# Performance work log

Measured on AMD Instinct MI355X. Metric: run time of the kernel, lower is better.

The kernel has to match this reference:

```python
import jax, jax.numpy as jnp
import numpy as np

DIM = 512
NUM_HEADS = 8


def setup_inputs() -> dict:
    key = jax.random.key(0)
    k1, k2, k3, k4, k5 = jax.random.split(key, 5)
    B, N, C = 4, 4096, DIM
    x = jax.random.normal(k1, (B, N, C), dtype=jnp.float32)
    # Conv1d kernel_size=1 weights, squeezed to [out, in]
    qkv_w = jax.random.normal(k2, (3 * C, C), dtype=jnp.float32) * (C ** -0.5)
    qkv_b = jax.random.normal(k3, (3 * C,), dtype=jnp.float32) * 0.02
    out_w = jax.random.normal(k4, (C, C), dtype=jnp.float32) * (C ** -0.5)
    out_b = jax.random.normal(k5, (C,), dtype=jnp.float32) * 0.02
    return {"x": x, "qkv_w": qkv_w, "qkv_b": qkv_b, "out_w": out_w, "out_b": out_b}


def reference(x, qkv_w, qkv_b, out_w, out_b):
    B, N, C = x.shape
    H = NUM_HEADS
    hd = C // H
    scale = hd ** -0.5
    # 1x1 Conv1d == per-position linear: [B,N,C] x [3C,C] -> [B,N,3C]
    qkv = jnp.einsum('bnc,oc->bno', x, qkv_w) + qkv_b
    qkv = qkv.reshape(B, N, 3, H, hd)
    q, k, v = qkv[:, :, 0], qkv[:, :, 1], qkv[:, :, 2]  # each [B,N,H,hd]
    # NOTE: faithful to the original: q @ k.transpose(-2,-1) contracts head_dim
    # giving an [B,N,H,H] score matrix (attention across heads per position).
    scores = jnp.einsum('bnhd,bngd->bnhg', q, k) * scale
    attn = jax.nn.softmax(scores, axis=-1)
    out = jnp.einsum('bnhg,bngd->bnhd', attn, v)  # [B,N,H,hd]
    # Faithful to original: transpose(1,2) then reshape(B,N,C) interleaves axes.
    out = out.transpose(0, 2, 1, 3).reshape(B, N, C)
    out = jnp.einsum('bnc,oc->bno', out, out_w) + out_b
    return out
```

## Files before the change

kernel.cpp:

```cpp
#include <hip/hip_runtime.h>
#include <hip/hip_bf16.h>

#define DIMC 512
#define SEQ 4096
#define M_TOK 16384
#define N_QKV 1536

typedef __bf16 bfv8 __attribute__((ext_vector_type(8)));
typedef float f32v4 __attribute__((ext_vector_type(4)));
typedef unsigned short u16v8 __attribute__((ext_vector_type(8)));

static __device__ __forceinline__ float bf2f(unsigned short u) {
    union { unsigned int i; float f; } x; x.i = ((unsigned int)u) << 16; return x.f;
}
static __device__ __forceinline__ unsigned short f2bf(float f) {
    union { float f; unsigned int i; } x; x.f = f;
    unsigned int r = x.i + 0x7FFFu + ((x.i >> 16) & 1u);
    return (unsigned short)(r >> 16);
}

static __device__ __forceinline__ void gload_lds16(const void* g, void* s) {
    __builtin_amdgcn_global_load_lds(
        (const __attribute__((address_space(1))) unsigned int*)g,
        (__attribute__((address_space(3))) unsigned int*)s, 16, 0, 0);
}

#define NX8  (M_TOK * DIMC / 8)
#define NWQ8 (N_QKV * DIMC / 8)
#define NWO8 (DIMC * DIMC / 8)
__global__ __launch_bounds__(256) void cvt_all(
    const float* __restrict__ x,  const float* __restrict__ wq,
    const float* __restrict__ wo, unsigned short* __restrict__ xb,
    unsigned short* __restrict__ wqb, unsigned short* __restrict__ wob)
{
    int i = blockIdx.x * 256 + threadIdx.x;
    const float* src; unsigned short* dst; int off;
    if (i < NX8)             { src = x;  dst = xb;  off = i; }
    else if (i < NX8 + NWQ8) { src = wq; dst = wqb; off = i - NX8; }
    else                     { src = wo; dst = wob; off = i - NX8 - NWQ8; }
    const float4* p = (const float4*)src + (size_t)off * 2;
    float4 a = p[0], b = p[1];
    u16v8 o;
    o[0] = f2bf(a.x); o[1] = f2bf(a.y); o[2] = f2bf(a.z); o[3] = f2bf(a.w);
    o[4] = f2bf(b.x); o[5] = f2bf(b.y); o[6] = f2bf(b.z); o[7] = f2bf(b.w);
    *(u16v8*)(dst + (size_t)off * 8) = o;
}

template<bool OUT_BF16>
__global__ __launch_bounds__(256) void gemm_nt_2ph(
    const unsigned short* __restrict__ A,
    const unsigned short* __restrict__ B,
    const float* __restrict__ bias,
    void* __restrict__ Cout,
    int M, int N, int K)
{
    __shared__ __align__(16) unsigned short As[2][128 * 32];
    __shared__ __align__(16) unsigned short Bs[2][128 * 32];
    const int tid  = threadIdx.x;
    const int lane = tid & 63;
    const int wid  = tid >> 6;
    const int wm   = wid >> 1;
    const int wn   = wid & 1;
    const int m0 = blockIdx.x * 128;
    const int n0 = blockIdx.y * 128;
    const int frow = lane & 15;
    const int fcol = (lane >> 4) * 8;
    const int NT = K >> 5;

    f32v4 acc[4][4] = {};

    const unsigned short* aSrc[2];
    const unsigned short* bSrc[2];
    #pragma unroll
    for (int s = 0; s < 2; ++s) {
        const int p   = (s * 256 + tid) * 8;
        const int row = p >> 5;
        const int col = (p & 31) ^ (((row >> 1) & 3) << 3);
        aSrc[s] = A + (size_t)(m0 + row) * K + col;
        bSrc[s] = B + (size_t)(n0 + row) * K + col;
    }
    const int dstOff[2] = { wid * 512, 2048 + wid * 512 };

#define STAGE(kt, buf)                                                         \
    {                                                                          \
        _Pragma("unroll") for (int s = 0; s < 2; ++s) {                        \
            gload_lds16(aSrc[s] + (kt) * 32, &As[buf][dstOff[s]]);             \
            gload_lds16(bSrc[s] + (kt) * 32, &Bs[buf][dstOff[s]]);             \
        }                                                                      \
    }

    STAGE(0, 0)
    __syncthreads();

    for (int t = 0; t < NT; ++t) {
        const int p = t & 1;
        if (t + 1 < NT) STAGE(t + 1, p ^ 1)
        bfv8 af[4], bf[4];
        #pragma unroll
        for (int i = 0; i < 4; ++i) {
            const int r = wm * 64 + i * 16 + frow;
            af[i] = *(const bfv8*)(&As[p][r * 32 + (fcol ^ (((r >> 1) & 3) << 3))]);
        }
        #pragma unroll
        for (int j = 0; j < 4; ++j) {
            const int r = wn * 64 + j * 16 + frow;
            bf[j] = *(const bfv8*)(&Bs[p][r * 32 + (fcol ^ (((r >> 1) & 3) << 3))]);
        }
        #pragma unroll
        for (int i = 0; i < 4; ++i)
            #pragma unroll
            for (int j = 0; j < 4; ++j)
                acc[i][j] = __builtin_amdgcn_mfma_f32_16x16x32_bf16(
                    af[i], bf[j], acc[i][j], 0, 0, 0);
        __syncthreads();
    }
#undef STAGE

    const int erow = (lane >> 4) * 4;
    const int ecol = lane & 15;
    #pragma unroll
    for (int j = 0; j < 4; ++j) {
        const int col = n0 + wn * 64 + j * 16 + ecol;
        const float bv = bias[col];
        #pragma unroll
        for (int i = 0; i < 4; ++i) {
            const int rbase = m0 + wm * 64 + i * 16 + erow;
            #pragma unroll
            for (int r = 0; r < 4; ++r) {
                const float v = acc[i][j][r] + bv;
                if constexpr (OUT_BF16)
                    ((unsigned short*)Cout)[(size_t)(rbase + r) * N + col] = f2bf(v);
                else
                    ((float*)Cout)[(size_t)(rbase + r) * N + col] = v;
            }
        }
    }
}

__global__ __launch_bounds__(256) void attn_mix2(
    const unsigned short* __restrict__ Y1,
    unsigned short* __restrict__ Y2)
{
    const int tid  = threadIdx.x;
    const int tok  = blockIdx.x * 16 + (tid >> 4);
    const int l16  = tid & 15;
    const int h    = l16 >> 1;
    const int half = l16 & 1;
    const unsigned short* qkv = Y1 + (size_t)tok * N_QKV;

    float qf[32];
    #pragma unroll
    for (int c = 0; c < 4; ++c) {
        u16v8 v = *(const u16v8*)(qkv + h * 64 + half * 32 + c * 8);
        #pragma unroll
        for (int j = 0; j < 8; ++j) qf[c * 8 + j] = bf2f(v[j]);
    }
    float sc[8];
    #pragma unroll
    for (int g = 0; g < 8; ++g) {
        const unsigned short* kp = qkv + DIMC + g * 64 + half * 32;
        float a = 0.f;
        #pragma unroll
        for (int c = 0; c < 4; ++c) {
            u16v8 v = *(const u16v8*)(kp + c * 8);
            #pragma unroll
            for (int j = 0; j < 8; ++j) a = fmaf(qf[c * 8 + j], bf2f(v[j]), a);
        }
        a += __shfl_xor(a, 1);
        sc[g] = a * 0.125f;
    }
    float mx = sc[0];
    #pragma unroll
    for (int g = 1; g < 8; ++g) mx = fmaxf(mx, sc[g]);
    float sum = 0.f;
    #pragma unroll
    for (int g = 0; g < 8; ++g) { sc[g] = __expf(sc[g] - mx); sum += sc[g]; }
    const float inv = 1.f / sum;
    #pragma unroll
    for (int g = 0; g < 8; ++g) sc[g] *= inv;

    float o[32] = {};
    #pragma unroll
    for (int g = 0; g < 8; ++g) {
        const unsigned short* vp = qkv + 2 * DIMC + g * 64 + half * 32;
        #pragma unroll
        for (int c = 0; c < 4; ++c) {
            u16v8 v = *(const u16v8*)(vp + c * 8);
            #pragma unroll
            for (int j = 0; j < 8; ++j) o[c * 8 + j] = fmaf(sc[g], bf2f(v[j]), o[c * 8 + j]);
        }
    }
    const int n = tok & (SEQ - 1);
    const int b = tok >> 12;
    const size_t drow = (size_t)b * SEQ + h * 512 + (n >> 3);
    unsigned short* dst = Y2 + drow * DIMC + ((n & 7) << 6) + half * 32;
    #pragma unroll
    for (int c = 0; c < 4; ++c) {
        u16v8 ov;
        #pragma unroll
        for (int j = 0; j < 8; ++j) ov[j] = f2bf(o[c * 8 + j]);
        *(u16v8*)(dst + c * 8) = ov;
    }
}

extern "C" void kernel_launch(void* const* d_in, const int* in_sizes, int n_in,
                              void* d_out, int out_size, void* d_ws, size_t ws_size,
                              hipStream_t stream) {
    const float* x     = (const float*)d_in[0];
    const float* qkv_w = (const float*)d_in[1];
    const float* qkv_b = (const float*)d_in[2];
    const float* out_w = (const float*)d_in[3];
    const float* out_b = (const float*)d_in[4];
    float* out = (float*)d_out;

    unsigned short* Y1 = (unsigned short*)d_ws;
    unsigned short* Xb = Y1 + (size_t)M_TOK * N_QKV;
    unsigned short* Y2 = Xb;
    unsigned short* Wq = Xb + (size_t)M_TOK * DIMC;
    unsigned short* Wo = Wq + (size_t)N_QKV * DIMC;

    cvt_all<<<(NX8 + NWQ8 + NWO8) / 256, 256, 0, stream>>>(x, qkv_w, out_w, Xb, Wq, Wo);

    gemm_nt_2ph<true><<<dim3(M_TOK / 128, N_QKV / 128), 256, 0, stream>>>(
        Xb, Wq, qkv_b, Y1, M_TOK, N_QKV, DIMC);

    attn_mix2<<<M_TOK / 16, 256, 0, stream>>>(Y1, Y2);

    gemm_nt_2ph<false><<<dim3(M_TOK / 128, DIMC / 128), 256, 0, stream>>>(
        Y2, Wo, out_b, out, M_TOK, DIMC, DIMC);
}
```

Before: 83.98 us.

## Use 128x256 GEMM tiles with 512 threads and triple-buffered LDS pipeline

Widens each GEMM block to a 128x256 output tile with 8 waves, which raises B-tile reuse per A load. The double-buffered LDS loop becomes a three-slot ring that prefetches two k-steps ahead. The full __syncthreads is replaced by explicit vmcnt/lgkmcnt waits plus s_barrier, so global-to-LDS loads overlap MFMA work. In exchange it uses more LDS per block and launches fewer blocks (the out-projection grid shrinks to 256 blocks), which risks lower occupancy and poorer load balance.

```diff
diff --git a/kernel.cpp b/kernel.cpp
--- a/kernel.cpp
+++ b/kernel.cpp
@@ -9,6 +9,9 @@
 typedef __bf16 bfv8 __attribute__((ext_vector_type(8)));
 typedef float f32v4 __attribute__((ext_vector_type(4)));
 typedef unsigned short u16v8 __attribute__((ext_vector_type(8)));
+
+#define VMCNT(n) asm volatile("s_waitcnt vmcnt(" #n ")" ::: "memory")
+#define LGKM0()  asm volatile("s_waitcnt lgkmcnt(0)" ::: "memory")
 
 static __device__ __forceinline__ float bf2f(unsigned short u) {
     union { unsigned int i; float f; } x; x.i = ((unsigned int)u) << 16; return x.f;
@@ -47,72 +50,78 @@
 }
 
 template<bool OUT_BF16>
-__global__ __launch_bounds__(256) void gemm_nt_2ph(
+__global__ __launch_bounds__(512) void gemm_nt_r3(
     const unsigned short* __restrict__ A,
     const unsigned short* __restrict__ B,
     const float* __restrict__ bias,
     void* __restrict__ Cout,
     int M, int N, int K)
 {
-    __shared__ __align__(16) unsigned short As[2][128 * 32];
-    __shared__ __align__(16) unsigned short Bs[2][128 * 32];
+    __shared__ __align__(16) unsigned short As[3][128 * 32];
+    __shared__ __align__(16) unsigned short Bs[3][256 * 32];
     const int tid  = threadIdx.x;
     const int lane = tid & 63;
     const int wid  = tid >> 6;
-    const int wm   = wid >> 1;
-    const int wn   = wid & 1;
+    const int wm   = wid >> 2;
+    const int wn   = wid & 3;
     const int m0 = blockIdx.x * 128;
-    const int n0 = blockIdx.y * 128;
+    const int n0 = blockIdx.y * 256;
     const int frow = lane & 15;
     const int fcol = (lane >> 4) * 8;
     const int NT = K >> 5;
 
     f32v4 acc[4][4] = {};
 
-    const unsigned short* aSrc[2];
+    const int arow = tid >> 2;
+    const int acol = ((tid & 3) * 8) ^ (((arow >> 1) & 3) << 3);
+    const unsigned short* aSrc = A + (size_t)(m0 + arow) * K + acol;
     const unsigned short* bSrc[2];
     #pragma unroll
-    for (int s = 0; s < 2; ++s) {
-        const int p   = (s * 256 + tid) * 8;
-        const int row = p >> 5;
-        const int col = (p & 31) ^ (((row >> 1) & 3) << 3);
-        aSrc[s] = A + (size_t)(m0 + row) * K + col;
-        bSrc[s] = B + (size_t)(n0 + row) * K + col;
-    }
-    const int dstOff[2] = { wid * 512, 2048 + wid * 512 };
-
-#define STAGE(kt, buf)                                                         \
+    for (int r = 0; r < 2; ++r) {
+        const int brow = r * 128 + (tid >> 2);
+        const int bcol = ((tid & 3) * 8) ^ (((brow >> 1) & 3) << 3);
+        bSrc[r] = B + (size_t)(n0 + brow) * K + bcol;
+    }
+    const int aDst = wid * 512;
+
+#define STAGE(kt, slot)                                                        \
     {                                                                          \
-        _Pragma("unroll") for (int s = 0; s < 2; ++s) {                        \
-            gload_lds16(aSrc[s] + (kt) * 32, &As[buf][dstOff[s]]);             \
-            gload_lds16(bSrc[s] + (kt) * 32, &Bs[buf][dstOff[s]]);             \
-        }                                                                      \
+        gload_lds16(aSrc + (kt) * 32, &As[slot][aDst]);                        \
+        gload_lds16(bSrc[0] + (kt) * 32, &Bs[slot][aDst]);                     \
+        gload_lds16(bSrc[1] + (kt) * 32, &Bs[slot][4096 + aDst]);              \
     }
 
     STAGE(0, 0)
-    __syncthreads();
+    STAGE(1, 1)
+    VMCNT(3);
+    __builtin_amdgcn_s_barrier();
 
     for (int t = 0; t < NT; ++t) {
-        const int p = t & 1;
-        if (t + 1 < NT) STAGE(t + 1, p ^ 1)
+        const int slot = t % 3;
         bfv8 af[4], bf[4];
         #pragma unroll
         for (int i = 0; i < 4; ++i) {
             const int r = wm * 64 + i * 16 + frow;
-            af[i] = *(const bfv8*)(&As[p][r * 32 + (fcol ^ (((r >> 1) & 3) << 3))]);
+            af[i] = *(const bfv8*)(&As[slot][r * 32 + (fcol ^ (((r >> 1) & 3) << 3))]);
         }
         #pragma unroll
         for (int j = 0; j < 4; ++j) {
             const int r = wn * 64 + j * 16 + frow;
-            bf[j] = *(const bfv8*)(&Bs[p][r * 32 + (fcol ^ (((r >> 1) & 3) << 3))]);
-        }
+            bf[j] = *(const bfv8*)(&Bs[slot][r * 32 + (fcol ^ (((r >> 1) & 3) << 3))]);
+        }
+        if (t + 2 < NT) {
+            const int ws = (t + 2) % 3;
+            STAGE(t + 2, ws)
+        }
+        LGKM0(); __builtin_amdgcn_sched_barrier(0);
         #pragma unroll
         for (int i = 0; i < 4; ++i)
             #pragma unroll
             for (int j = 0; j < 4; ++j)
                 acc[i][j] = __builtin_amdgcn_mfma_f32_16x16x32_bf16(
                     af[i], bf[j], acc[i][j], 0, 0, 0);
-        __syncthreads();
+        if (t + 2 < NT) { VMCNT(3); } else { VMCNT(0); }
+        __builtin_amdgcn_s_barrier();
     }
 #undef STAGE
 
@@ -221,11 +230,11 @@
 
     cvt_all<<<(NX8 + NWQ8 + NWO8) / 256, 256, 0, stream>>>(x, qkv_w, out_w, Xb, Wq, Wo);
 
-    gemm_nt_2ph<true><<<dim3(M_TOK / 128, N_QKV / 128), 256, 0, stream>>>(
+    gemm_nt_r3<true><<<dim3(M_TOK / 128, N_QKV / 256), 512, 0, stream>>>(
         Xb, Wq, qkv_b, Y1, M_TOK, N_QKV, DIMC);
 
     attn_mix2<<<M_TOK / 16, 256, 0, stream>>>(Y1, Y2);
 
-    gemm_nt_2ph<false><<<dim3(M_TOK / 128, DIMC / 128), 256, 0, stream>>>(
+    gemm_nt_r3<false><<<dim3(M_TOK / 128, DIMC / 256), 512, 0, stream>>>(
         Y2, Wo, out_b, out, M_TOK, DIMC, DIMC);
 }
```

After: 81.15 us. 3.4% less time.
